# Kernel tuning notes

Measured on AMD Instinct MI355X. Metric: run time of the kernel, lower is better.

Reference implementation:

```python
import jax, jax.numpy as jnp
import numpy as np

Q = 10        # icosahedral diamonds
M = 128       # 2**dggrid_level
L = Q * M * M # 163840 icosahedral points
KS = 9        # kernel_size / knn neighbors


def setup_inputs() -> dict:
    key = jax.random.key(0)
    k1, k2, k3, k4 = jax.random.split(key, 4)
    b, c, h, w = 1, 128, 256, 512
    x = jax.random.normal(k1, (b, c, h, w), dtype=jnp.float32)
    codeskmin = jax.random.randint(k2, (L, KS), 0, h * w, dtype=jnp.int32)
    att_w = jax.random.normal(k3, (KS, 2, KS), dtype=jnp.float32) * 0.1
    att_b = jnp.zeros((KS,), dtype=jnp.float32)
    depth_w = jax.random.normal(k4, (c, KS), dtype=jnp.float32) * 0.1
    depth_b = jnp.zeros((c,), dtype=jnp.float32)
    gamma = jnp.ones((c,), dtype=jnp.float32)
    beta = jnp.zeros((c,), dtype=jnp.float32)
    return {"x": x, "codeskmin": codeskmin, "att_w": att_w, "att_b": att_b,
            "depth_w": depth_w, "depth_b": depth_b, "gamma": gamma, "beta": beta}


def reference(x, codeskmin, att_w, att_b, depth_w, depth_b, gamma, beta):
    b, c, h, w = x.shape
    xf = x.reshape(b, c, h * w)
    # KNN gather: (b, c, L, KS)
    xe = xf[:, :, codeskmin]
    # --- SpatialAttentionModule_v1 ---
    avg = jnp.mean(xe, axis=1)           # (b, L, KS)
    mx = jnp.max(xe, axis=1)             # (b, L, KS)
    feat = jnp.stack([avg, mx], axis=1)  # (b, 2, L, KS)
    # Conv2d(2 -> KS, kernel (1,KS), no pad): reduces neighbor axis fully
    att = jnp.einsum('bilk,oik->bol', feat, att_w) + att_b[None, :, None]  # (b, KS, L)
    att = jax.nn.sigmoid(att)
    att = att.transpose(0, 2, 1)[:, None, :, :]  # (b, 1, L, KS)
    xe = att * xe + xe
    # --- depthwise conv over neighbor axis ---
    out = jnp.einsum('bclk,ck->bcl', xe, depth_w) + depth_b[None, :, None]  # (b, c, L)
    # rearrange 'b c (q h w) -> (b q) c h w'
    out = out.reshape(b, c, Q, M, M).transpose(0, 2, 1, 3, 4).reshape(b * Q, c, M, M)
    # BatchNorm (training-mode batch stats)
    mean = jnp.mean(out, axis=(0, 2, 3), keepdims=True)
    var = jnp.var(out, axis=(0, 2, 3), keepdims=True)
    out = (out - mean) * jax.lax.rsqrt(var + 1e-5)
    out = out * gamma[None, :, None, None] + beta[None, :, None, None]
    # Swish
    out = out * jax.nn.sigmoid(out)
    return out
```

## Files before the change

kernel.cpp:

```cpp
#include <hip/hip_runtime.h>
#include <hip/hip_bf16.h>

#define HW 131072
#define NCH 128
#define KS 9
#define L_TOTAL 163840
#define NGRP 8
#define LPB 256

typedef float        f32x2 __attribute__((ext_vector_type(2)));
typedef float        f32x4 __attribute__((ext_vector_type(4)));
typedef unsigned int u32x2 __attribute__((ext_vector_type(2)));
typedef unsigned int u32x4 __attribute__((ext_vector_type(4)));

static __device__ __forceinline__ float bflo(unsigned int p) { return __uint_as_float(p << 16); }
static __device__ __forceinline__ float bfhi(unsigned int p) { return __uint_as_float(p & 0xffff0000u); }
static __device__ __forceinline__ unsigned short f2bf(float f) {
    unsigned int x = __float_as_uint(f);
    return (unsigned short)((x + 0x7fffu + ((x >> 16) & 1u)) >> 16);
}
static __device__ __forceinline__ unsigned int pack2(float a, float b) {
    return (unsigned int)f2bf(a) | ((unsigned int)f2bf(b) << 16);
}

__global__ __launch_bounds__(256) void transpose_x_kernel(
    const f32x2* __restrict__ xf,
    unsigned int* __restrict__ xT,
    float2* __restrict__ meanmaxP)
{
    __shared__ unsigned short tile[128 * 128];
    __shared__ float ps[4][128];
    __shared__ float pm[4][128];
    const int tid = threadIdx.x;
    const int lane = tid & 63;
    const int wave = tid >> 6;
    const int p0 = blockIdx.x * 128;
    const int pa = 2 * lane, pb = 2 * lane + 1;

    float s0 = 0.f, s1 = 0.f;
    float m0 = -3.4e38f, m1 = -3.4e38f;
    #pragma unroll 8
    for (int it = 0; it < 32; ++it) {
        int c = wave + (it << 2);
        f32x2 v = __builtin_nontemporal_load(&xf[(long)c * (HW / 2) + (p0 >> 1) + lane]);
        tile[pa * 128 + ((c + 2 * pa) & 127)] = f2bf(v.x);
        tile[pb * 128 + ((c + 2 * pb) & 127)] = f2bf(v.y);
        s0 += v.x; s1 += v.y;
        m0 = fmaxf(m0, v.x); m1 = fmaxf(m1, v.y);
    }
    ps[wave][pa] = s0; ps[wave][pb] = s1;
    pm[wave][pa] = m0; pm[wave][pb] = m1;
    __syncthreads();

    #pragma unroll 8
    for (int it = 0; it < 32; ++it) {
        int p = wave + (it << 2);
        int colr = (2 * lane + 2 * p) & 127;
        unsigned int d = *reinterpret_cast<const unsigned int*>(&tile[p * 128 + colr]);
        xT[((long)(lane >> 3) * HW + (p0 + p)) * 8 + (lane & 7)] = d;
    }
    if (tid < 128) {
        float s = ps[0][tid] + ps[1][tid] + ps[2][tid] + ps[3][tid];
        float m = fmaxf(fmaxf(pm[0][tid], pm[1][tid]), fmaxf(pm[2][tid], pm[3][tid]));
        meanmaxP[p0 + tid] = make_float2(s * 0.0078125f, m);
    }
}

__global__ __launch_bounds__(256) void mult_kernel(
    const float2* __restrict__ meanmaxP,
    const int* __restrict__ cks,
    const float* __restrict__ att_w,
    const float* __restrict__ att_b,
    unsigned int* __restrict__ rec)
{
    __shared__ float attw[162];
    __shared__ float attb[12];
    __shared__ int lcks[64 * 12];
    const int tid = threadIdx.x;
    const int base_l = blockIdx.x * 64;

    if (tid < 162) attw[tid] = att_w[tid];
    if (tid < KS) attb[tid] = att_b[tid];
    for (int j = tid; j < 64 * KS; j += 256) {
        const int lj = j / KS;
        lcks[lj * 12 + (j - lj * KS)] = cks[(long)base_l * KS + j];
    }
    __syncthreads();

    const int l_local = tid >> 2;
    const int sub = tid & 3;
    if (sub < 3) {
        float mean[KS], mx[KS];
        #pragma unroll
        for (int k = 0; k < KS; ++k) {
            float2 mm = meanmaxP[lcks[l_local * 12 + k]];
            mean[k] = mm.x; mx[k] = mm.y;
        }
        #pragma unroll
        for (int oo = 0; oo < 3; ++oo) {
            int o = sub * 3 + oo;
            float logit = attb[o];
            #pragma unroll
            for (int k = 0; k < KS; ++k) {
                logit = fmaf(mean[k], attw[o * 18 + k], logit);
                logit = fmaf(mx[k],   attw[o * 18 + 9 + k], logit);
            }
            float sig = 1.0f / (1.0f + __expf(-logit));
            unsigned int u = (unsigned int)(sig * 32768.0f + 0.5f);
            if (u > 32767u) u = 32767u;
            rec[(long)(base_l + l_local) * 12 + o] =
                (unsigned int)lcks[l_local * 12 + o] | (u << 17);
        }
    }
}

__global__ __launch_bounds__(256, 4) void gather_kernel(
    const unsigned int* __restrict__ xT,
    const unsigned int* __restrict__ rec,
    const float* __restrict__ depth_w,
    const float* __restrict__ depth_b,
    unsigned int* __restrict__ ybuf,
    float* __restrict__ gsum, float* __restrict__ gsq)
{
    __shared__ float dwl[KS][16];
    __shared__ float dbl[16];
    __shared__ float redx[4][4][8];

    const int tid  = threadIdx.x;
    const int lane = tid & 63;
    const int wave = tid >> 6;
    const int g      = blockIdx.x & 7;
    const int base_l = (blockIdx.x >> 3) * LPB;
    const int qt = lane & 3;
    const int lq = lane >> 2;

    if (tid < 144) {
        int k = tid >> 4, ch = tid & 15;
        dwl[k][ch] = depth_w[(g * 16 + ch) * KS + k];
    }
    if (tid < 16) dbl[tid] = depth_b[g * 16 + tid];
    __syncthreads();

    f32x2 dw[KS][2];
    #pragma unroll
    for (int k = 0; k < KS; ++k) {
        f32x4 t = *(const f32x4*)&dwl[k][qt * 4];
        dw[k][0].x = t.x; dw[k][0].y = t.y;
        dw[k][1].x = t.z; dw[k][1].y = t.w;
    }
    f32x2 db01, db23;
    {
        f32x4 t = *(const f32x4*)&dbl[qt * 4];
        db01.x = t.x; db01.y = t.y; db23.x = t.z; db23.y = t.w;
    }

    const unsigned int* slab = xT + ((size_t)g << 20);
    const int LH = L_TOTAL / 2;
    unsigned int* yb = ybuf + (size_t)(g * 16 + qt * 4) * LH + (base_l >> 1);

    f32x2 sum01 = {0.f, 0.f}, sum23 = {0.f, 0.f};
    f32x2 sq01  = {0.f, 0.f}, sq23  = {0.f, 0.f};

    #pragma unroll
    for (int b = 0; b < 2; ++b) {
        const int lw = wave * 64 + b * 32 + 2 * lq;
        const unsigned int* rp = rec + (size_t)(base_l + lw) * 12;
        const u32x4 a0 = __builtin_nontemporal_load((const u32x4*)rp);
        const u32x4 a1 = __builtin_nontemporal_load((const u32x4*)(rp + 4));
        const unsigned int a8 = __builtin_nontemporal_load(rp + 8);
        const u32x4 c0 = __builtin_nontemporal_load((const u32x4*)(rp + 12));
        const u32x4 c1 = __builtin_nontemporal_load((const u32x4*)(rp + 16));
        const unsigned int c8 = __builtin_nontemporal_load(rp + 20);
        const unsigned int rA[KS] = {a0.x, a0.y, a0.z, a0.w,
                                     a1.x, a1.y, a1.z, a1.w, a8};
        const unsigned int rB[KS] = {c0.x, c0.y, c0.z, c0.w,
                                     c1.x, c1.y, c1.z, c1.w, c8};

        u32x2 pA[KS], pB[KS];
        #pragma unroll
        for (int k = 0; k < KS; ++k)
            pA[k] = *(const u32x2*)(slab + ((rA[k] & 0x1FFFFu) << 3) + (qt << 1));
        #pragma unroll
        for (int k = 0; k < KS; ++k)
            pB[k] = *(const u32x2*)(slab + ((rB[k] & 0x1FFFFu) << 3) + (qt << 1));

        f32x2 aA01 = db01, aA23 = db23, aB01 = db01, aB23 = db23;
        #pragma unroll
        for (int k = 0; k < KS; ++k) {
            const float mA = fmaf((float)(rA[k] >> 17), 3.0517578125e-5f, 1.0f);
            f32x2 mA2; mA2.x = mA; mA2.y = mA;
            f32x2 xa; xa.x = bflo(pA[k].x); xa.y = bfhi(pA[k].x);
            f32x2 xb; xb.x = bflo(pA[k].y); xb.y = bfhi(pA[k].y);
            aA01 = __builtin_elementwise_fma(xa * mA2, dw[k][0], aA01);
            aA23 = __builtin_elementwise_fma(xb * mA2, dw[k][1], aA23);
            const float mB = fmaf((float)(rB[k] >> 17), 3.0517578125e-5f, 1.0f);
            f32x2 mB2; mB2.x = mB; mB2.y = mB;
            f32x2 ya; ya.x = bflo(pB[k].x); ya.y = bfhi(pB[k].x);
            f32x2 ybv; ybv.x = bflo(pB[k].y); ybv.y = bfhi(pB[k].y);
            aB01 = __builtin_elementwise_fma(ya * mB2, dw[k][0], aB01);
            aB23 = __builtin_elementwise_fma(ybv * mB2, dw[k][1], aB23);
        }

        const int pi = wave * 32 + b * 16 + lq;
        yb[0 * LH + pi] = pack2(aA01.x, aB01.x);
        yb[1 * LH + pi] = pack2(aA01.y, aB01.y);
        yb[2 * LH + pi] = pack2(aA23.x, aB23.x);
        yb[3 * LH + pi] = pack2(aA23.y, aB23.y);

        sum01 += aA01 + aB01; sum23 += aA23 + aB23;
        sq01 = __builtin_elementwise_fma(aA01, aA01, sq01);
        sq01 = __builtin_elementwise_fma(aB01, aB01, sq01);
        sq23 = __builtin_elementwise_fma(aA23, aA23, sq23);
        sq23 = __builtin_elementwise_fma(aB23, aB23, sq23);
    }

    #pragma unroll
    for (int s = 4; s <= 32; s <<= 1) {
        sum01.x += __shfl_xor(sum01.x, s);
        sum01.y += __shfl_xor(sum01.y, s);
        sum23.x += __shfl_xor(sum23.x, s);
        sum23.y += __shfl_xor(sum23.y, s);
        sq01.x  += __shfl_xor(sq01.x,  s);
        sq01.y  += __shfl_xor(sq01.y,  s);
        sq23.x  += __shfl_xor(sq23.x,  s);
        sq23.y  += __shfl_xor(sq23.y,  s);
    }
    if (lane < 4) {
        float* rw = &redx[wave][lane][0];
        rw[0] = sum01.x; rw[1] = sum01.y; rw[2] = sum23.x; rw[3] = sum23.y;
        rw[4] = sq01.x;  rw[5] = sq01.y;  rw[6] = sq23.x;  rw[7] = sq23.y;
    }
    __syncthreads();
    if (tid < 32) {
        const int q = tid >> 2, qq = tid & 3;
        float s = redx[0][qq][q] + redx[1][qq][q] + redx[2][qq][q] + redx[3][qq][q];
        const int ch = g * 16 + qq * 4 + (q & 3);
        float* dst = (q >= 4) ? gsq : gsum;
        atomicAdd(&dst[ch], s);
    }
}

__global__ __launch_bounds__(256) void finalize_kernel(
    const u32x4* __restrict__ ybuf,
    const float* __restrict__ gsum, const float* __restrict__ gsq,
    const float* __restrict__ gamma, const float* __restrict__ beta,
    float* __restrict__ out)
{
    const int q = blockIdx.x >> 7;
    const int c = blockIdx.x & 127;
    const int tid = threadIdx.x;

    const float invN = 1.0f / (float)L_TOTAL;
    const float m = gsum[c] * invN;
    const float var = gsq[c] * invN - m * m;
    const float sc = gamma[c] * rsqrtf(var + 1e-5f);
    const float sh = beta[c] - m * sc;

    const u32x4* src = ybuf + (size_t)c * (L_TOTAL / 8) + (size_t)q * 2048;
    float* dst = out + ((size_t)(q * NCH + c) << 14);

    #pragma unroll 2
    for (int it = 0; it < 8; ++it) {
        const int i = it * 256 + tid;
        const u32x4 v = src[i];
        f32x4 o0, o1;
        float z;
        z = fmaf(bflo(v.x), sc, sh); o0.x = z / (1.0f + __expf(-z));
        z = fmaf(bfhi(v.x), sc, sh); o0.y = z / (1.0f + __expf(-z));
        z = fmaf(bflo(v.y), sc, sh); o0.z = z / (1.0f + __expf(-z));
        z = fmaf(bfhi(v.y), sc, sh); o0.w = z / (1.0f + __expf(-z));
        z = fmaf(bflo(v.z), sc, sh); o1.x = z / (1.0f + __expf(-z));
        z = fmaf(bfhi(v.z), sc, sh); o1.y = z / (1.0f + __expf(-z));
        z = fmaf(bflo(v.w), sc, sh); o1.z = z / (1.0f + __expf(-z));
        z = fmaf(bfhi(v.w), sc, sh); o1.w = z / (1.0f + __expf(-z));
        *(f32x4*)&dst[i * 8 + 0] = o0;
        *(f32x4*)&dst[i * 8 + 4] = o1;
    }
}

extern "C" void kernel_launch(void* const* d_in, const int* in_sizes, int n_in,
                              void* d_out, int out_size, void* d_ws, size_t ws_size,
                              hipStream_t stream) {
    const f32x2* x_f2  = (const f32x2*)d_in[0];
    const int* cks     = (const int*)d_in[1];
    const float* aw    = (const float*)d_in[2];
    const float* ab    = (const float*)d_in[3];
    const float* dw    = (const float*)d_in[4];
    const float* db    = (const float*)d_in[5];
    const float* gm    = (const float*)d_in[6];
    const float* bt    = (const float*)d_in[7];

    char* ws = (char*)d_ws;
    unsigned int* xT   = (unsigned int*)ws;
    float2* meanmaxP   = (float2*)(ws + 33554432);
    unsigned int* ybuf = (unsigned int*)(ws + 34603008);
    unsigned int* rec  = (unsigned int*)(ws + 76546048);
    float* gsum        = (float*)(ws + 84410368);
    float* gsq         = gsum + NCH;

    hipMemsetAsync(gsum, 0, 2 * NCH * sizeof(float), stream);

    transpose_x_kernel<<<HW / 128, 256, 0, stream>>>(x_f2, xT, meanmaxP);
    mult_kernel<<<L_TOTAL / 64, 256, 0, stream>>>(meanmaxP, cks, aw, ab, rec);
    gather_kernel<<<(L_TOTAL / LPB) * NGRP, 256, 0, stream>>>(
        xT, rec, dw, db, ybuf, gsum, gsq);
    finalize_kernel<<<1280, 256, 0, stream>>>(
        (const u32x4*)ybuf, gsum, gsq, gm, bt, (float*)d_out);
}
```

Before: 307.0 us.

## Stage gather outputs in LDS for coalesced stores, fold memset into mult kernel

The gather kernel now processes one point per quad per iteration over four iterations, writes bf16 results into a shared-memory tile, and after a barrier stores each channel row with wide 16-byte coalesced writes. Previously it interleaved two points and did scattered 4-byte stores. The transpose kernel's write loop is remapped so consecutive threads write contiguous xT segments. The memset of the stats accumulators is removed and done by block 0 of mult_kernel, saving one launch. The cost is extra LDS use and a barrier in the gather kernel, plus less memory-level parallelism per iteration in the gathers.

```diff
diff --git a/kernel.cpp b/kernel.cpp
--- a/kernel.cpp
+++ b/kernel.cpp
@@ -18,9 +18,6 @@
 static __device__ __forceinline__ unsigned short f2bf(float f) {
     unsigned int x = __float_as_uint(f);
     return (unsigned short)((x + 0x7fffu + ((x >> 16) & 1u)) >> 16);
-}
-static __device__ __forceinline__ unsigned int pack2(float a, float b) {
-    return (unsigned int)f2bf(a) | ((unsigned int)f2bf(b) << 16);
 }
 
 __global__ __launch_bounds__(256) void transpose_x_kernel(
@@ -54,10 +51,15 @@
 
     #pragma unroll 8
     for (int it = 0; it < 32; ++it) {
-        int p = wave + (it << 2);
-        int colr = (2 * lane + 2 * p) & 127;
-        unsigned int d = *reinterpret_cast<const unsigned int*>(&tile[p * 128 + colr]);
-        xT[((long)(lane >> 3) * HW + (p0 + p)) * 8 + (lane & 7)] = d;
+        int idx = it * 256 + tid;
+        int s = idx >> 10;
+        int rem = idx & 1023;
+        int p = rem >> 3;
+        int d = rem & 7;
+        int cpair = s * 8 + d;
+        unsigned int u = *reinterpret_cast<const unsigned int*>(
+            &tile[p * 128 + ((2 * cpair + 2 * p) & 127)]);
+        xT[((long)s * HW + (p0 + p)) * 8 + d] = u;
     }
     if (tid < 128) {
         float s = ps[0][tid] + ps[1][tid] + ps[2][tid] + ps[3][tid];
@@ -71,13 +73,16 @@
     const int* __restrict__ cks,
     const float* __restrict__ att_w,
     const float* __restrict__ att_b,
-    unsigned int* __restrict__ rec)
+    unsigned int* __restrict__ rec,
+    float* __restrict__ gz)
 {
     __shared__ float attw[162];
     __shared__ float attb[12];
     __shared__ int lcks[64 * 12];
     const int tid = threadIdx.x;
     const int base_l = blockIdx.x * 64;
+
+    if (blockIdx.x == 0) gz[tid] = 0.f;
 
     if (tid < 162) attw[tid] = att_w[tid];
     if (tid < KS) attb[tid] = att_b[tid];
@@ -125,6 +130,7 @@
     __shared__ float dwl[KS][16];
     __shared__ float dbl[16];
     __shared__ float redx[4][4][8];
+    __shared__ __align__(16) unsigned short ytile[16][264];
 
     const int tid  = threadIdx.x;
     const int lane = tid & 63;
@@ -155,63 +161,57 @@
     }
 
     const unsigned int* slab = xT + ((size_t)g << 20);
-    const int LH = L_TOTAL / 2;
-    unsigned int* yb = ybuf + (size_t)(g * 16 + qt * 4) * LH + (base_l >> 1);
 
     f32x2 sum01 = {0.f, 0.f}, sum23 = {0.f, 0.f};
     f32x2 sq01  = {0.f, 0.f}, sq23  = {0.f, 0.f};
 
     #pragma unroll
-    for (int b = 0; b < 2; ++b) {
-        const int lw = wave * 64 + b * 32 + 2 * lq;
-        const unsigned int* rp = rec + (size_t)(base_l + lw) * 12;
-        const u32x4 a0 = __builtin_nontemporal_load((const u32x4*)rp);
-        const u32x4 a1 = __builtin_nontemporal_load((const u32x4*)(rp + 4));
-        const unsigned int a8 = __builtin_nontemporal_load(rp + 8);
-        const u32x4 c0 = __builtin_nontemporal_load((const u32x4*)(rp + 12));
-        const u32x4 c1 = __builtin_nontemporal_load((const u32x4*)(rp + 16));
-        const unsigned int c8 = __builtin_nontemporal_load(rp + 20);
-        const unsigned int rA[KS] = {a0.x, a0.y, a0.z, a0.w,
-                                     a1.x, a1.y, a1.z, a1.w, a8};
-        const unsigned int rB[KS] = {c0.x, c0.y, c0.z, c0.w,
-                                     c1.x, c1.y, c1.z, c1.w, c8};
-
-        u32x2 pA[KS], pB[KS];
+    for (int b = 0; b < 4; ++b) {
+        const int lloc = wave * 64 + b * 16 + lq;
+        const unsigned int* rp = rec + (size_t)(base_l + lloc) * 12;
+        const u32x4 r0 = __builtin_nontemporal_load((const u32x4*)rp);
+        const u32x4 r1 = __builtin_nontemporal_load((const u32x4*)(rp + 4));
+        const unsigned int r8 = __builtin_nontemporal_load(rp + 8);
+        const unsigned int rr[KS] = {r0.x, r0.y, r0.z, r0.w,
+                                     r1.x, r1.y, r1.z, r1.w, r8};
+
+        u32x2 pv[KS];
         #pragma unroll
         for (int k = 0; k < KS; ++k)
-            pA[k] = *(const u32x2*)(slab + ((rA[k] & 0x1FFFFu) << 3) + (qt << 1));
-        #pragma unroll
-        for (int k = 0; k < KS; ++k)
-            pB[k] = *(const u32x2*)(slab + ((rB[k] & 0x1FFFFu) << 3) + (qt << 1));
-
-        f32x2 aA01 = db01, aA23 = db23, aB01 = db01, aB23 = db23;
+            pv[k] = *(const u32x2*)(slab + ((rr[k] & 0x1FFFFu) << 3) + (qt << 1));
+
+        f32x2 acc01 = db01, acc23 = db23;
         #pragma unroll
         for (int k = 0; k < KS; ++k) {
-            const float mA = fmaf((float)(rA[k] >> 17), 3.0517578125e-5f, 1.0f);
-            f32x2 mA2; mA2.x = mA; mA2.y = mA;
-            f32x2 xa; xa.x = bflo(pA[k].x); xa.y = bfhi(pA[k].x);
-            f32x2 xb; xb.x = bflo(pA[k].y); xb.y = bfhi(pA[k].y);
-            aA01 = __builtin_elementwise_fma(xa * mA2, dw[k][0], aA01);
-            aA23 = __builtin_elementwise_fma(xb * mA2, dw[k][1], aA23);
-            const float mB = fmaf((float)(rB[k] >> 17), 3.0517578125e-5f, 1.0f);
-            f32x2 mB2; mB2.x = mB; mB2.y = mB;
-            f32x2 ya; ya.x = bflo(pB[k].x); ya.y = bfhi(pB[k].x);
-            f32x2 ybv; ybv.x = bflo(pB[k].y); ybv.y = bfhi(pB[k].y);
-            aB01 = __builtin_elementwise_fma(ya * mB2, dw[k][0], aB01);
-            aB23 = __builtin_elementwise_fma(ybv * mB2, dw[k][1], aB23);
+            const float mk = fmaf((float)(rr[k] >> 17), 3.0517578125e-5f, 1.0f);
+            f32x2 mk2; mk2.x = mk; mk2.y = mk;
+            f32x2 xa; xa.x = bflo(pv[k].x); xa.y = bfhi(pv[k].x);
+            f32x2 xb; xb.x = bflo(pv[k].y); xb.y = bfhi(pv[k].y);
+            acc01 = __builtin_elementwise_fma(xa * mk2, dw[k][0], acc01);
+            acc23 = __builtin_elementwise_fma(xb * mk2, dw[k][1], acc23);
         }
 
-        const int pi = wave * 32 + b * 16 + lq;
-        yb[0 * LH + pi] = pack2(aA01.x, aB01.x);
-        yb[1 * LH + pi] = pack2(aA01.y, aB01.y);
-        yb[2 * LH + pi] = pack2(aA23.x, aB23.x);
-        yb[3 * LH + pi] = pack2(aA23.y, aB23.y);
-
-        sum01 += aA01 + aB01; sum23 += aA23 + aB23;
-        sq01 = __builtin_elementwise_fma(aA01, aA01, sq01);
-        sq01 = __builtin_elementwise_fma(aB01, aB01, sq01);
-        sq23 = __builtin_elementwise_fma(aA23, aA23, sq23);
-        sq23 = __builtin_elementwise_fma(aB23, aB23, sq23);
+        ytile[qt * 4 + 0][lloc] = f2bf(acc01.x);
+        ytile[qt * 4 + 1][lloc] = f2bf(acc01.y);
+        ytile[qt * 4 + 2][lloc] = f2bf(acc23.x);
+        ytile[qt * 4 + 3][lloc] = f2bf(acc23.y);
+
+        sum01 += acc01; sum23 += acc23;
+        sq01 = __builtin_elementwise_fma(acc01, acc01, sq01);
+        sq23 = __builtin_elementwise_fma(acc23, acc23, sq23);
+    }
+
+    __syncthreads();
+
+    {
+        const int ch = tid >> 4;
+        const int m  = tid & 15;
+        const u32x4 v0 = *(const u32x4*)&ytile[ch][m * 16];
+        const u32x4 v1 = *(const u32x4*)&ytile[ch][m * 16 + 8];
+        unsigned int* dst = ybuf + (size_t)(g * 16 + ch) * (L_TOTAL / 2)
+                          + (base_l >> 1) + m * 8;
+        *(u32x4*)dst = v0;
+        *(u32x4*)(dst + 4) = v1;
     }
 
     #pragma unroll
@@ -298,10 +298,8 @@
     float* gsum        = (float*)(ws + 84410368);
     float* gsq         = gsum + NCH;
 
-    hipMemsetAsync(gsum, 0, 2 * NCH * sizeof(float), stream);
-
     transpose_x_kernel<<<HW / 128, 256, 0, stream>>>(x_f2, xT, meanmaxP);
-    mult_kernel<<<L_TOTAL / 64, 256, 0, stream>>>(meanmaxP, cks, aw, ab, rec);
+    mult_kernel<<<L_TOTAL / 64, 256, 0, stream>>>(meanmaxP, cks, aw, ab, rec, gsum);
     gather_kernel<<<(L_TOTAL / LPB) * NGRP, 256, 0, stream>>>(
         xT, rec, dw, db, ybuf, gsum, gsq);
     finalize_kernel<<<1280, 256, 0, stream>>>(
```

New measurement: 280.7 us. 1.09x faster.
